# Optimization experiments

Measured on AMD Instinct MI355X. Metric: run time of the kernel, lower is better.

## Reference

```python
import jax, jax.numpy as jnp
import numpy as np


def bilinear_align_corners(p, H, W):
    # p: [B, C, h, w] -> [B, C, H, W], matches F.interpolate(mode='bilinear', align_corners=True)
    b, c, h, w = p.shape
    ys = jnp.linspace(0.0, h - 1.0, H)
    xs = jnp.linspace(0.0, w - 1.0, W)
    y0 = jnp.floor(ys).astype(jnp.int32)
    x0 = jnp.floor(xs).astype(jnp.int32)
    y1 = jnp.minimum(y0 + 1, h - 1)
    x1 = jnp.minimum(x0 + 1, w - 1)
    wy = (ys - y0.astype(p.dtype))[:, None]          # [H,1]
    wx = (xs - x0.astype(p.dtype))                   # [W]
    rows = p[:, :, y0, :] * (1 - wy) + p[:, :, y1, :] * wy   # [B,C,H,w]
    out = rows[:, :, :, x0] * (1 - wx) + rows[:, :, :, x1] * wx  # [B,C,H,W]
    return out


def conv1x1(x, W, b):
    return jnp.einsum('bchw,oc->bohw', x, W) + b[None, :, None, None]


def scan_axis(feat, A_bar, B_bar, axis):
    # selective recurrence h_i = A_i * stop_grad(h_{i-1}) + B_i * x_i along `axis`
    f = jnp.moveaxis(feat, axis, 0)
    A = jnp.moveaxis(A_bar, axis, 0)
    B = jnp.moveaxis(B_bar, axis, 0)

    def step(prev, inp):
        a_i, b_i, x_i = inp
        h = a_i * jax.lax.stop_gradient(prev) + b_i * x_i
        return h, h

    _, hs = jax.lax.scan(step, jnp.zeros_like(f[0]), (A, B, f))
    return jnp.moveaxis(hs, 0, axis)


def setup_inputs() -> dict:
    key = jax.random.key(0)
    ks = jax.random.split(key, 12)
    Bsz, Cin, H, W = 4, 64, 256, 256
    hid = 128
    s_in = 1.0 / np.sqrt(Cin)
    s_hid = 1.0 / np.sqrt(hid)
    return {
        'x': jax.random.normal(ks[0], (Bsz, Cin, H, W), jnp.float32),
        'prior': jax.random.normal(ks[1], (Bsz, 1, 64, 64), jnp.float32),
        'W_in': jax.random.uniform(ks[2], (hid, Cin), jnp.float32, -s_in, s_in),
        'b_in': jax.random.uniform(ks[3], (hid,), jnp.float32, -s_in, s_in),
        'W_out': jax.random.uniform(ks[4], (Cin, hid), jnp.float32, -s_hid, s_hid),
        'b_out': jax.random.uniform(ks[5], (Cin,), jnp.float32, -s_hid, s_hid),
        'W_delta': jax.random.uniform(ks[6], (hid, hid), jnp.float32, -s_hid, s_hid),
        'b_delta': jax.random.uniform(ks[7], (hid,), jnp.float32, -s_hid, s_hid),
        'W_B': jax.random.uniform(ks[8], (hid, hid), jnp.float32, -s_hid, s_hid),
        'b_B': jax.random.uniform(ks[9], (hid,), jnp.float32, -s_hid, s_hid),
        'A_param': jax.random.normal(ks[10], (hid,), jnp.float32),
        'lambda_delta': jnp.float32(0.1),
        'alpha': jnp.float32(0.1),
        'gamma': jnp.float32(0.1),
    }


def reference(x, prior, W_in, b_in, W_out, b_out, W_delta, b_delta, W_B, b_B,
              A_param, lambda_delta, alpha, gamma):
    Bsz, C, H, W = x.shape
    prior_up = jnp.clip(bilinear_align_corners(prior, H, W), -1.0, 1.0)
    x_proj = conv1x1(x, W_in, b_in)
    delta = jax.nn.softplus(conv1x1(x_proj, W_delta, b_delta) + lambda_delta * prior_up)
    B_k = conv1x1(x_proj, W_B, b_B) * (1.0 + alpha * prior_up)
    A = -jnp.exp(A_param)[None, :, None, None]
    A_bar = jnp.exp(delta * A)
    B_bar = delta * B_k
    # dim=0 in torch code scans along W (axis 3); dim=1 scans along H (axis 2)
    scanned = scan_axis(x_proj, A_bar, B_bar, 3) + scan_axis(x_proj, A_bar, B_bar, 2)
    out = conv1x1(scanned, W_out, b_out)
    return (x + gamma * out, prior_up)
```

## Files before the change

### kernel.cpp

```cpp
#include <hip/hip_runtime.h>
#include <hip/hip_bf16.h>

#define OUT1 16777216
#define BIG  33554432

typedef _Float16 half8 __attribute__((ext_vector_type(8)));
typedef float    floatx4 __attribute__((ext_vector_type(4)));

struct __align__(8) h4s { _Float16 x, y, z, w; };
__device__ inline void store4h(_Float16* p, float4 v){
    h4s t; t.x = (_Float16)v.x; t.y = (_Float16)v.y; t.z = (_Float16)v.z; t.w = (_Float16)v.w;
    *(h4s*)p = t;
}

__global__ __launch_bounds__(256) void k_prior(const float* __restrict__ prior, float* __restrict__ pu){
    int i = blockIdx.x*256 + threadIdx.x;
    int b = i >> 16;
    int rem = i & 65535;
    int yy = rem >> 8, xx = rem & 255;
    const float scale = 63.0f/255.0f;
    float sy = yy*scale, sx = xx*scale;
    int y0 = min((int)floorf(sy), 63), x0 = min((int)floorf(sx), 63);
    int y1 = min(y0+1, 63), x1 = min(x0+1, 63);
    float wy = sy - (float)y0, wx = sx - (float)x0;
    const float* pb = prior + (b<<12);
    float v00 = pb[(y0<<6)+x0], v01 = pb[(y0<<6)+x1];
    float v10 = pb[(y1<<6)+x0], v11 = pb[(y1<<6)+x1];
    float r0 = v00*(1.f-wy) + v10*wy;
    float r1 = v01*(1.f-wy) + v11*wy;
    float v  = r0*(1.f-wx) + r1*wx;
    pu[i] = fminf(fmaxf(v, -1.f), 1.f);
}

__global__ __launch_bounds__(256) void k_comb(const float* __restrict__ W_in, const float* __restrict__ b_in,
        const float* __restrict__ W_delta, const float* __restrict__ b_delta,
        const float* __restrict__ W_B, const float* __restrict__ b_B,
        const float* __restrict__ A_param, const float* __restrict__ W_out,
        _Float16* __restrict__ Wch, float* __restrict__ bcv, float* __restrict__ negA,
        _Float16* __restrict__ Wof){
    int i = blockIdx.x*256 + threadIdx.x;
    if (i < 24576){
        int r = i >> 6, c = i & 63;
        float v;
        if (r < 128) v = W_in[i];
        else if (r < 256){
            int rr = r-128; float s = 0.f;
            for (int k=0;k<128;k++) s = fmaf(W_delta[(rr<<7)+k], W_in[(k<<6)+c], s);
            v = s;
        } else {
            int rr = r-256; float s = 0.f;
            for (int k=0;k<128;k++) s = fmaf(W_B[(rr<<7)+k], W_in[(k<<6)+c], s);
            v = s;
        }
        Wch[i] = (_Float16)v;
    } else if (i < 24960){
        int r = i - 24576; float v;
        if (r < 128) v = b_in[r];
        else if (r < 256){
            int rr=r-128; float s = b_delta[rr];
            for (int k=0;k<128;k++) s = fmaf(W_delta[(rr<<7)+k], b_in[k], s);
            v = s;
        } else {
            int rr=r-256; float s = b_B[rr];
            for (int k=0;k<128;k++) s = fmaf(W_B[(rr<<7)+k], b_in[k], s);
            v = s;
        }
        bcv[r] = v;
    } else if (i < 25088){
        negA[i-24960] = -expf(A_param[i-24960]);
    } else if (i < 33280){
        Wof[i-25088] = (_Float16)W_out[i-25088];
    }
}

__global__ __launch_bounds__(256, 2) void k_proj_mfma(const float* __restrict__ x, const float* __restrict__ pu,
        const _Float16* __restrict__ Wch, const float* __restrict__ bcv, const float* __restrict__ negA,
        const float* __restrict__ lam_p, const float* __restrict__ alp_p,
        _Float16* __restrict__ Ab, _Float16* __restrict__ Uu){
    __shared__ _Float16 Ws[384][72];

    const int t    = threadIdx.x;
    const int lane = t & 63;
    const int wave = t >> 6;
    const int col  = lane & 15;
    const int quad = lane >> 4;

    const int blk = blockIdx.x;
    const int b   = blk >> 10;
    const int p0  = (blk & 1023) << 6;
    const int pxw = p0 + (wave << 4);

    {
        const float4* wsrc = (const float4*)Wch;
        #pragma unroll
        for (int i = 0; i < 12; i++){
            int c = t + i*256;
            int row = c >> 3, part = c & 7;
            float4 v = wsrc[c];
            *(float4*)&Ws[row][part<<3] = v;
        }
    }

    const float* xb = x + ((size_t)b<<22) + pxw + col;
    half8 aX[2];
    #pragma unroll
    for (int kh = 0; kh < 2; kh++){
        half8 h;
        #pragma unroll
        for (int j = 0; j < 8; j++){
            int k = kh*32 + quad*8 + j;
            h[j] = (_Float16)xb[(size_t)k<<16];
        }
        aX[kh] = h;
    }
    __syncthreads();

    floatx4 acc[24];
    #pragma unroll
    for (int nt = 0; nt < 24; nt++){
        half8 b0 = *(const half8*)&Ws[nt*16 + col][quad*8];
        half8 b1 = *(const half8*)&Ws[nt*16 + col][32 + quad*8];
        floatx4 a = (floatx4){0.f,0.f,0.f,0.f};
        a = __builtin_amdgcn_mfma_f32_16x16x32_f16(aX[0], b0, a, 0, 0, 0);
        a = __builtin_amdgcn_mfma_f32_16x16x32_f16(aX[1], b1, a, 0, 0, 0);
        acc[nt] = a;
    }

    const float lamv = lam_p[0], alpv = alp_p[0];
    float4 puv4 = *(const float4*)(pu + (b<<16) + pxw + (quad<<2));
    float lpu[4], apu[4];
    #pragma unroll
    for (int r = 0; r < 4; r++){
        float pv = ((const float*)&puv4)[r];
        lpu[r] = lamv * pv;
        apu[r] = fmaf(alpv, pv, 1.f);
    }
    #pragma unroll
    for (int ct = 0; ct < 8; ct++){
        int c = (ct<<4) + col;
        float bI = bcv[c], bD = bcv[128+c], bB = bcv[256+c], nA = negA[c];
        floatx4 aI = acc[ct], aD = acc[8+ct], aB = acc[16+ct];
        h4s oa, ou;
        #pragma unroll
        for (int r = 0; r < 4; r++){
            float sI = aI[r] + bI;
            float sD = aD[r] + bD;
            float sB = aB[r] + bB;
            float dpre  = sD + lpu[r];
            float delta = fmaxf(dpre, 0.f) + __logf(1.f + __expf(-fabsf(dpre)));
            float ab    = __expf(nA * delta);
            float uu    = delta * sB * apu[r] * sI;
            (&oa.x)[r] = (_Float16)ab;
            (&ou.x)[r] = (_Float16)uu;
        }
        size_t o = ((size_t)((b<<7) + c)<<16) + pxw + (quad<<2);
        *(h4s*)(Ab+o) = oa;
        *(h4s*)(Uu+o) = ou;
    }
}

__global__ __launch_bounds__(256) void k_scan_w(const _Float16* __restrict__ Ab, const _Float16* __restrict__ Uu,
                                                _Float16* __restrict__ Sw){
    int r    = (blockIdx.x<<2) + (threadIdx.x>>6);
    int lane = threadIdx.x & 63;
    size_t base = ((size_t)r<<8) + (lane<<2);
    h4s a4 = *(const h4s*)(Ab+base);
    h4s u4 = *(const h4s*)(Uu+base);
    float ax=(float)a4.x, ay=(float)a4.y, az=(float)a4.z, aw=(float)a4.w;
    float ux=(float)u4.x, uy=(float)u4.y, uz=(float)u4.z, uw=(float)u4.w;
    float A = ax, U = ux;
    U = fmaf(ay, U, uy); A *= ay;
    U = fmaf(az, U, uz); A *= az;
    U = fmaf(aw, U, uw); A *= aw;
    #pragma unroll
    for (int off=1; off<64; off<<=1){
        float Apv = __shfl_up(A, off, 64);
        float Upv = __shfl_up(U, off, 64);
        if (lane >= off){ U = fmaf(A, Upv, U); A *= Apv; }
    }
    float h = __shfl_up(U, 1, 64);
    if (lane == 0) h = 0.f;
    float4 o;
    h = fmaf(ax, h, ux); o.x = h;
    h = fmaf(ay, h, uy); o.y = h;
    h = fmaf(az, h, uz); o.z = h;
    h = fmaf(aw, h, uw); o.w = h;
    store4h(Sw+base, o);
}

__global__ __launch_bounds__(256) void k_scan_h(const _Float16* __restrict__ AbH, const _Float16* __restrict__ UuH,
                                                const _Float16* __restrict__ Sw, _Float16* __restrict__ Sh){
    int t   = blockIdx.x*256 + threadIdx.x;
    int col = t >> 8;
    int w   = t & 255;
    size_t base = ((size_t)col<<16) + w;
    float h = 0.f;
    #pragma unroll 4
    for (int hh=0; hh<256; hh++){
        size_t idx = base + ((size_t)hh<<8);
        float a = (float)AbH[idx];
        float u = (float)UuH[idx];
        float s = (float)Sw[idx];
        h = fmaf(a, h, u);
        Sh[idx] = (_Float16)(h + s);
    }
}

__global__ __launch_bounds__(256, 2) void k_out_mfma(const float* __restrict__ x, const _Float16* __restrict__ Sh,
        const _Float16* __restrict__ Wof, const float* __restrict__ bout, const float* __restrict__ gam_p,
        float* __restrict__ out){
    const int t    = threadIdx.x;
    const int lane = t & 63;
    const int wave = t >> 6;
    const int col  = lane & 15;
    const int quad = lane >> 4;
    const int b    = blockIdx.x >> 8;
    const int p0   = (blockIdx.x & 255) << 8;
    const int wn0  = wave << 6;

    const _Float16* shb = Sh + ((size_t)b<<23) + p0;

    floatx4 acc[4][4];
    #pragma unroll
    for (int mt = 0; mt < 4; mt++)
        #pragma unroll
        for (int nt = 0; nt < 4; nt++)
            acc[mt][nt] = (floatx4){0.f,0.f,0.f,0.f};

    #pragma unroll
    for (int kc = 0; kc < 4; kc++){
        half8 bf[4];
        #pragma unroll
        for (int nt = 0; nt < 4; nt++){
            int px = wn0 + nt*16 + col;
            #pragma unroll
            for (int j = 0; j < 8; j++)
                bf[nt][j] = shb[((size_t)(kc*32 + quad*8 + j)<<16) + px];
        }
        half8 af[4];
        #pragma unroll
        for (int mt = 0; mt < 4; mt++)
            af[mt] = *(const half8*)(Wof + (mt*16 + col)*128 + kc*32 + quad*8);
        #pragma unroll
        for (int mt = 0; mt < 4; mt++)
            #pragma unroll
            for (int nt = 0; nt < 4; nt++)
                acc[mt][nt] = __builtin_amdgcn_mfma_f32_16x16x32_f16(af[mt], bf[nt], acc[mt][nt], 0, 0, 0);
    }

    const float gv = gam_p[0];
    #pragma unroll
    for (int mt = 0; mt < 4; mt++){
        #pragma unroll
        for (int nt = 0; nt < 4; nt++){
            int px = wn0 + nt*16 + col;
            #pragma unroll
            for (int r = 0; r < 4; r++){
                int o = mt*16 + quad*4 + r;
                size_t idx = (((size_t)(b*64 + o))<<16) + p0 + px;
                out[idx] = fmaf(gv, acc[mt][nt][r] + bout[o], x[idx]);
            }
        }
    }
}

extern "C" void kernel_launch(void* const* d_in, const int* in_sizes, int n_in,
                              void* d_out, int out_size, void* d_ws, size_t ws_size,
                              hipStream_t stream){
    const float* x       = (const float*)d_in[0];
    const float* prior   = (const float*)d_in[1];
    const float* W_in    = (const float*)d_in[2];
    const float* b_in    = (const float*)d_in[3];
    const float* W_out   = (const float*)d_in[4];
    const float* b_out   = (const float*)d_in[5];
    const float* W_delta = (const float*)d_in[6];
    const float* b_delta = (const float*)d_in[7];
    const float* W_B     = (const float*)d_in[8];
    const float* b_B     = (const float*)d_in[9];
    const float* A_param = (const float*)d_in[10];
    const float* lam     = (const float*)d_in[11];
    const float* alp     = (const float*)d_in[12];
    const float* gam     = (const float*)d_in[13];

    float* out = (float*)d_out;
    float* pu  = out + OUT1;

    float* ws        = (float*)d_ws;
    _Float16* Wch    = (_Float16*)ws;
    float* bcv       = ws + 12288;
    float* negA      = ws + 12672;
    _Float16* Wof    = (_Float16*)(ws + 12800);
    _Float16* AbH    = (_Float16*)(ws + 32768);
    _Float16* UuH    = AbH + BIG;
    _Float16* Sh     = UuH + BIG;
    _Float16* Sw     = (_Float16*)out;

    hipLaunchKernelGGL(k_prior,  dim3(1024),  dim3(256), 0, stream, prior, pu);
    hipLaunchKernelGGL(k_comb,   dim3(130),   dim3(256), 0, stream, W_in, b_in, W_delta, b_delta,
                       W_B, b_B, A_param, W_out, Wch, bcv, negA, Wof);
    hipLaunchKernelGGL(k_proj_mfma, dim3(4096), dim3(256), 0, stream,
                       x, pu, Wch, bcv, negA, lam, alp, AbH, UuH);
    hipLaunchKernelGGL(k_scan_w, dim3(32768), dim3(256), 0, stream, AbH, UuH, Sw);
    hipLaunchKernelGGL(k_scan_h, dim3(512),   dim3(256), 0, stream, AbH, UuH, Sw, Sh);
    hipLaunchKernelGGL(k_out_mfma, dim3(1024), dim3(256), 0, stream, x, Sh, Wof, b_out, gam, out);
}
```

Baseline: 323.5 us.

## Fuse W and H scans into one per-plane kernel and drop LDS weight staging

Merges the separate W-direction and H-direction scan kernels into a single kernel. One 64-lane wave per channel plane walks the rows, doing a wave-level prefix scan along W and carrying per-column H recurrences in registers. This removes the fp16 Sw intermediate write and re-read and one kernel launch. The projection kernel also stops staging weights in LDS and reads them straight from global or cache, with higher occupancy bounds. The risk is that the fused scan runs only 512 single-wave blocks that each do 256 sequential steps of shuffle work, which may leave much of the GPU idle and make the scan latency-bound.

```diff
diff --git a/kernel.cpp b/kernel.cpp
--- a/kernel.cpp
+++ b/kernel.cpp
@@ -73,12 +73,10 @@
     }
 }
 
-__global__ __launch_bounds__(256, 2) void k_proj_mfma(const float* __restrict__ x, const float* __restrict__ pu,
+__global__ __launch_bounds__(256, 4) void k_proj_mfma(const float* __restrict__ x, const float* __restrict__ pu,
         const _Float16* __restrict__ Wch, const float* __restrict__ bcv, const float* __restrict__ negA,
         const float* __restrict__ lam_p, const float* __restrict__ alp_p,
         _Float16* __restrict__ Ab, _Float16* __restrict__ Uu){
-    __shared__ _Float16 Ws[384][72];
-
     const int t    = threadIdx.x;
     const int lane = t & 63;
     const int wave = t >> 6;
@@ -90,17 +88,6 @@
     const int p0  = (blk & 1023) << 6;
     const int pxw = p0 + (wave << 4);
 
-    {
-        const float4* wsrc = (const float4*)Wch;
-        #pragma unroll
-        for (int i = 0; i < 12; i++){
-            int c = t + i*256;
-            int row = c >> 3, part = c & 7;
-            float4 v = wsrc[c];
-            *(float4*)&Ws[row][part<<3] = v;
-        }
-    }
-
     const float* xb = x + ((size_t)b<<22) + pxw + col;
     half8 aX[2];
     #pragma unroll
@@ -112,18 +99,6 @@
             h[j] = (_Float16)xb[(size_t)k<<16];
         }
         aX[kh] = h;
-    }
-    __syncthreads();
-
-    floatx4 acc[24];
-    #pragma unroll
-    for (int nt = 0; nt < 24; nt++){
-        half8 b0 = *(const half8*)&Ws[nt*16 + col][quad*8];
-        half8 b1 = *(const half8*)&Ws[nt*16 + col][32 + quad*8];
-        floatx4 a = (floatx4){0.f,0.f,0.f,0.f};
-        a = __builtin_amdgcn_mfma_f32_16x16x32_f16(aX[0], b0, a, 0, 0, 0);
-        a = __builtin_amdgcn_mfma_f32_16x16x32_f16(aX[1], b1, a, 0, 0, 0);
-        acc[nt] = a;
     }
 
     const float lamv = lam_p[0], alpv = alp_p[0];
@@ -135,17 +110,33 @@
         lpu[r] = lamv * pv;
         apu[r] = fmaf(alpv, pv, 1.f);
     }
+
     #pragma unroll
     for (int ct = 0; ct < 8; ct++){
         int c = (ct<<4) + col;
-        float bI = bcv[c], bD = bcv[128+c], bB = bcv[256+c], nA = negA[c];
-        floatx4 aI = acc[ct], aD = acc[8+ct], aB = acc[16+ct];
+        const _Float16* wI = Wch + ((size_t)c<<6)        + quad*8;
+        const _Float16* wD = Wch + ((size_t)(128+c)<<6)  + quad*8;
+        const _Float16* wB = Wch + ((size_t)(256+c)<<6)  + quad*8;
+        half8 bI0 = *(const half8*)wI,        bI1 = *(const half8*)(wI+32);
+        half8 bD0 = *(const half8*)wD,        bD1 = *(const half8*)(wD+32);
+        half8 bB0 = *(const half8*)wB,        bB1 = *(const half8*)(wB+32);
+        floatx4 aI = (floatx4){0.f,0.f,0.f,0.f};
+        floatx4 aD = (floatx4){0.f,0.f,0.f,0.f};
+        floatx4 aB = (floatx4){0.f,0.f,0.f,0.f};
+        aI = __builtin_amdgcn_mfma_f32_16x16x32_f16(aX[0], bI0, aI, 0, 0, 0);
+        aD = __builtin_amdgcn_mfma_f32_16x16x32_f16(aX[0], bD0, aD, 0, 0, 0);
+        aB = __builtin_amdgcn_mfma_f32_16x16x32_f16(aX[0], bB0, aB, 0, 0, 0);
+        aI = __builtin_amdgcn_mfma_f32_16x16x32_f16(aX[1], bI1, aI, 0, 0, 0);
+        aD = __builtin_amdgcn_mfma_f32_16x16x32_f16(aX[1], bD1, aD, 0, 0, 0);
+        aB = __builtin_amdgcn_mfma_f32_16x16x32_f16(aX[1], bB1, aB, 0, 0, 0);
+
+        float bIc = bcv[c], bDc = bcv[128+c], bBc = bcv[256+c], nA = negA[c];
         h4s oa, ou;
         #pragma unroll
         for (int r = 0; r < 4; r++){
-            float sI = aI[r] + bI;
-            float sD = aD[r] + bD;
-            float sB = aB[r] + bB;
+            float sI = aI[r] + bIc;
+            float sD = aD[r] + bDc;
+            float sB = aB[r] + bBc;
             float dpre  = sD + lpu[r];
             float delta = fmaxf(dpre, 0.f) + __logf(1.f + __expf(-fabsf(dpre)));
             float ab    = __expf(nA * delta);
@@ -159,50 +150,41 @@
     }
 }
 
-__global__ __launch_bounds__(256) void k_scan_w(const _Float16* __restrict__ Ab, const _Float16* __restrict__ Uu,
-                                                _Float16* __restrict__ Sw){
-    int r    = (blockIdx.x<<2) + (threadIdx.x>>6);
-    int lane = threadIdx.x & 63;
-    size_t base = ((size_t)r<<8) + (lane<<2);
-    h4s a4 = *(const h4s*)(Ab+base);
-    h4s u4 = *(const h4s*)(Uu+base);
-    float ax=(float)a4.x, ay=(float)a4.y, az=(float)a4.z, aw=(float)a4.w;
-    float ux=(float)u4.x, uy=(float)u4.y, uz=(float)u4.z, uw=(float)u4.w;
-    float A = ax, U = ux;
-    U = fmaf(ay, U, uy); A *= ay;
-    U = fmaf(az, U, uz); A *= az;
-    U = fmaf(aw, U, uw); A *= aw;
-    #pragma unroll
-    for (int off=1; off<64; off<<=1){
-        float Apv = __shfl_up(A, off, 64);
-        float Upv = __shfl_up(U, off, 64);
-        if (lane >= off){ U = fmaf(A, Upv, U); A *= Apv; }
-    }
-    float h = __shfl_up(U, 1, 64);
-    if (lane == 0) h = 0.f;
-    float4 o;
-    h = fmaf(ax, h, ux); o.x = h;
-    h = fmaf(ay, h, uy); o.y = h;
-    h = fmaf(az, h, uz); o.z = h;
-    h = fmaf(aw, h, uw); o.w = h;
-    store4h(Sw+base, o);
-}
-
-__global__ __launch_bounds__(256) void k_scan_h(const _Float16* __restrict__ AbH, const _Float16* __restrict__ UuH,
-                                                const _Float16* __restrict__ Sw, _Float16* __restrict__ Sh){
-    int t   = blockIdx.x*256 + threadIdx.x;
-    int col = t >> 8;
-    int w   = t & 255;
-    size_t base = ((size_t)col<<16) + w;
-    float h = 0.f;
+__global__ __launch_bounds__(64) void k_scan2(const _Float16* __restrict__ Ab, const _Float16* __restrict__ Uu,
+                                              _Float16* __restrict__ Sh){
+    const int plane = blockIdx.x;
+    const int lane  = threadIdx.x;
+    size_t pbase = ((size_t)plane<<16) + (lane<<2);
+    float h0=0.f, h1=0.f, h2=0.f, h3=0.f;
     #pragma unroll 4
-    for (int hh=0; hh<256; hh++){
-        size_t idx = base + ((size_t)hh<<8);
-        float a = (float)AbH[idx];
-        float u = (float)UuH[idx];
-        float s = (float)Sw[idx];
-        h = fmaf(a, h, u);
-        Sh[idx] = (_Float16)(h + s);
+    for (int hh = 0; hh < 256; hh++){
+        size_t base = pbase + ((size_t)hh<<8);
+        h4s a4 = *(const h4s*)(Ab+base);
+        h4s u4 = *(const h4s*)(Uu+base);
+        float ax=(float)a4.x, ay=(float)a4.y, az=(float)a4.z, aw=(float)a4.w;
+        float ux=(float)u4.x, uy=(float)u4.y, uz=(float)u4.z, uw=(float)u4.w;
+        float A = ax, U = ux;
+        U = fmaf(ay, U, uy); A *= ay;
+        U = fmaf(az, U, uz); A *= az;
+        U = fmaf(aw, U, uw); A *= aw;
+        #pragma unroll
+        for (int off=1; off<64; off<<=1){
+            float Apv = __shfl_up(A, off, 64);
+            float Upv = __shfl_up(U, off, 64);
+            if (lane >= off){ U = fmaf(A, Upv, U); A *= Apv; }
+        }
+        float hw = __shfl_up(U, 1, 64);
+        if (lane == 0) hw = 0.f;
+        h0 = fmaf(ax, h0, ux);
+        h1 = fmaf(ay, h1, uy);
+        h2 = fmaf(az, h2, uz);
+        h3 = fmaf(aw, h3, uw);
+        float4 o;
+        hw = fmaf(ax, hw, ux); o.x = hw + h0;
+        hw = fmaf(ay, hw, uy); o.y = hw + h1;
+        hw = fmaf(az, hw, uz); o.z = hw + h2;
+        hw = fmaf(aw, hw, uw); o.w = hw + h3;
+        store4h(Sh+base, o);
     }
 }
 
@@ -293,14 +275,12 @@
     _Float16* AbH    = (_Float16*)(ws + 32768);
     _Float16* UuH    = AbH + BIG;
     _Float16* Sh     = UuH + BIG;
-    _Float16* Sw     = (_Float16*)out;
 
     hipLaunchKernelGGL(k_prior,  dim3(1024),  dim3(256), 0, stream, prior, pu);
     hipLaunchKernelGGL(k_comb,   dim3(130),   dim3(256), 0, stream, W_in, b_in, W_delta, b_delta,
                        W_B, b_B, A_param, W_out, Wch, bcv, negA, Wof);
     hipLaunchKernelGGL(k_proj_mfma, dim3(4096), dim3(256), 0, stream,
                        x, pu, Wch, bcv, negA, lam, alp, AbH, UuH);
-    hipLaunchKernelGGL(k_scan_w, dim3(32768), dim3(256), 0, stream, AbH, UuH, Sw);
-    hipLaunchKernelGGL(k_scan_h, dim3(512),   dim3(256), 0, stream, AbH, UuH, Sw, Sh);
+    hipLaunchKernelGGL(k_scan2, dim3(512), dim3(64), 0, stream, AbH, UuH, Sh);
     hipLaunchKernelGGL(k_out_mfma, dim3(1024), dim3(256), 0, stream, x, Sh, Wof, b_out, gam, out);
 }
```

Result: slower. 362.0 us (+11.9%).
